# Kernel tuning notes

Hardware: AMD Instinct MI355X
Metric: run time of the kernel (lower is better)

The kernel has to match this reference:

```python
import jax, jax.numpy as jnp
import numpy as np

B, N_CGS, N_ATOMS, KNN, K, DEPTH = 16, 256, 1024, 32, 128, 3
CUTOFF = 10.0


def _init_params(key):
    ks = jax.random.split(key, 12)
    s = 1.0 / np.sqrt(K)
    p = {}
    # stacked per-depth settransform weights: Linear stored as [in, out] (y = x @ W + b)
    p['mlp_W1'] = jax.random.normal(ks[0], (DEPTH, K, K), jnp.float32) * s
    p['mlp_b1'] = jnp.zeros((DEPTH, K), jnp.float32)
    p['mlp_W2'] = jax.random.normal(ks[1], (DEPTH, K, K), jnp.float32) * s
    p['mlp_b2'] = jnp.zeros((DEPTH, K), jnp.float32)
    p['upd_W1'] = jax.random.normal(ks[2], (DEPTH, K, K), jnp.float32) * s
    p['upd_b1'] = jnp.zeros((DEPTH, K), jnp.float32)
    p['upd_W2'] = jax.random.normal(ks[3], (DEPTH, K, K), jnp.float32) * s
    p['upd_b2'] = jnp.zeros((DEPTH, K), jnp.float32)
    p['dec_W1'] = jax.random.normal(ks[4], (K, K), jnp.float32) * s
    p['dec_b1'] = jnp.zeros((K,), jnp.float32)
    p['dec_W2'] = jax.random.normal(ks[5], (K, N_ATOMS), jnp.float32) * s
    p['dec_b2'] = jnp.zeros((N_ATOMS,), jnp.float32)
    return p


def setup_inputs() -> dict:
    key = jax.random.key(0)
    ks = jax.random.split(key, 6)
    inp = {
        'soft_assign': jax.random.uniform(ks[0], (B, N_ATOMS, N_CGS), jnp.float32),
        'xyz': jax.random.normal(ks[1], (B, N_ATOMS, 3), jnp.float32),
        'cg_xyz': jax.random.normal(ks[2], (B, N_CGS, 3), jnp.float32),
        'assign_norm': jax.random.uniform(ks[3], (B, N_ATOMS, N_CGS), jnp.float32),
        'assign_idx': jax.random.randint(ks[4], (N_ATOMS,), 0, N_CGS, jnp.int32),
    }
    inp.update(_init_params(ks[5]))
    return inp


def _forward(cg_xyz, assign_norm, assign_idx,
             mlp_W1, mlp_b1, mlp_W2, mlp_b2,
             upd_W1, upd_b1, upd_W2, upd_b2,
             dec_W1, dec_b1, dec_W2, dec_b2):
    act = jax.nn.relu
    # Pairwise CG distance + ascending sort (as in source). The source then
    # zeroes sorted values beyond rank knn and uses value.nonzero()[:, 1:] as
    # neighbor pairs, i.e. it indexes by SORT RANK (ranks 1..knn), not by the
    # sorted index tensor knbrs. For generic (distinct) coordinates this is
    # exactly: neighbor j in {1..knn} for every center i. We replicate that.
    dist_vec = cg_xyz[:, None, 1:KNN + 1, :] - cg_xyz[:, :, None, :]  # [B, n_cgs, knn, 3]
    dist_vec = dist_vec.reshape(B, N_CGS * KNN, 3)
    dist = jnp.sqrt(jnp.sum(dist_vec ** 2, axis=-1)).reshape(B, N_CGS, KNN, 1)

    # GaussianSmearing(0, cutoff, feature_dim)
    offset = jnp.linspace(0.0, CUTOFF, K)  # [K]
    coeff = -0.5 / (offset[1] - offset[0]) ** 2
    out = jnp.exp(coeff * (dist - offset) ** 2)  # [B, n_cgs, knn, K]

    # settransform layers (loop over small fixed depth)
    for d in range(DEPTH):
        upd = act(out @ mlp_W1[d] + mlp_b1[d]) @ mlp_W2[d] + mlp_b2[d]
        cg_contract = jnp.mean(upd, axis=-2, keepdims=True)  # mean over knn axis
        h = upd + cg_contract
        out = act(h @ upd_W1[d] + upd_b1[d]) @ upd_W2[d] + upd_b2[d]

    # decode K -> n_atoms
    coeffs = (act(out @ dec_W1 + dec_b1) @ dec_W2 + dec_b2)
    coeffs = coeffs.reshape(B, N_CGS * KNN, N_ATOMS)

    dx_recon = jnp.einsum('bio,bin->bon', coeffs, dist_vec)      # [B, n_atoms, 3]
    cg_offset = jnp.einsum('bin,bij->bjn', dx_recon, assign_norm)  # [B, n_cgs, 3]
    cg_offset_lift = cg_offset[:, assign_idx, :]                  # [B, n_atoms, 3]
    xyz_recon = cg_xyz[:, assign_idx, :] - cg_offset_lift + dx_recon
    return xyz_recon


def reference(soft_assign, xyz, cg_xyz, assign_norm, assign_idx,
              mlp_W1, mlp_b1, mlp_W2, mlp_b2,
              upd_W1, upd_b1, upd_W2, upd_b2,
              dec_W1, dec_b1, dec_W2, dec_b2):
    xyz_recon = _forward(cg_xyz, assign_norm, assign_idx,
                         mlp_W1, mlp_b1, mlp_W2, mlp_b2,
                         upd_W1, upd_b1, upd_W2, upd_b2,
                         dec_W1, dec_b1, dec_W2, dec_b2)
    return (soft_assign, xyz, xyz_recon)
```

## Files before the change

kernel.cpp:

```cpp
#include <hip/hip_runtime.h>

#define BATCH   16
#define NCGS    256
#define NATOMS  1024
#define KNN     32
#define KF      128
#define NSLICE  8

typedef __attribute__((ext_vector_type(8))) short bf16x8;
typedef __attribute__((ext_vector_type(4))) float f32x4;

#define NFRAG (13*8*4)

union U16B { bf16x8 v; uint u[4]; };

__global__ __launch_bounds__(256)
void prep_kernel(const float* __restrict__ mlp_W1, const float* __restrict__ mlp_W2,
                 const float* __restrict__ upd_W1, const float* __restrict__ upd_W2,
                 const float* __restrict__ dec_W1, uint* __restrict__ Wswz)
{
    int t = blockIdx.x * 256 + threadIdx.x;
    if (t >= 13*8*4*64) return;
    int lane = t & 63;
    int kc   = (t >> 6) & 3;
    int ft   = (t >> 8) & 7;
    int s    = t >> 11;

    const float* W;
    if (s < 12) {
        int d = s >> 2, ph = s & 3;
        if      (ph == 0) W = mlp_W1 + d*KF*KF;
        else if (ph == 1) W = mlp_W2 + d*KF*KF;
        else if (ph == 2) W = upd_W1 + d*KF*KF;
        else              W = upd_W2 + d*KF*KF;
    } else W = dec_W1;

    int f = ft*16 + (lane & 15);
    int g = lane >> 4;

    uint hi[4], lo[4];
    #pragma unroll
    for (int w = 0; w < 4; ++w) {
        int k0;
        if (s == 0) k0 = kc*32 + g*8 + 2*w;
        else        k0 = kc*16 + (w>>1)*64 + g*4 + 2*(w&1);
        float v0 = W[(size_t)k0*KF + f];
        float v1 = W[(size_t)(k0+1)*KF + f];
        uint b0 = __float_as_uint(v0), b1 = __float_as_uint(v1);
        hi[w] = (b0 >> 16) | (b1 & 0xffff0000u);
        float l0 = v0 - __uint_as_float(b0 & 0xffff0000u);
        float l1 = v1 - __uint_as_float(b1 & 0xffff0000u);
        lo[w] = (__float_as_uint(l0) >> 16) | (__float_as_uint(l1) & 0xffff0000u);
    }
    int fi = (s*8 + ft)*4 + kc;
    uint* ph_ = Wswz + (size_t)((fi*2 + 0)*64 + lane)*4;
    uint* pl_ = Wswz + (size_t)((fi*2 + 1)*64 + lane)*4;
    #pragma unroll
    for (int w = 0; w < 4; ++w) { ph_[w] = hi[w]; pl_[w] = lo[w]; }
}

template<int KC, int FH>
__device__ __forceinline__ void loadw(bf16x8 (&wb)[8], const bf16x8* __restrict__ Ws, int l)
{
    #pragma unroll
    for (int i = 0; i < 4; ++i) {
        const int idx = ((FH*4 + i)*4 + KC)*2;
        wb[i*2+0] = Ws[(idx+0)*64 + l];
        wb[i*2+1] = Ws[(idx+1)*64 + l];
    }
}

template<int KC, int FH>
__device__ __forceinline__ void compw(const bf16x8 (&wb)[8],
        const bf16x8 (&bh)[2][4], const bf16x8 (&bl)[2][4], f32x4 (&acc)[8][2])
{
    #pragma unroll
    for (int i = 0; i < 4; ++i) {
        const int ft = FH*4 + i;
        bf16x8 whi = wb[i*2+0], wlo = wb[i*2+1];
        #pragma unroll
        for (int rt = 0; rt < 2; ++rt) {
            acc[ft][rt] = __builtin_amdgcn_mfma_f32_16x16x32_bf16(whi, bh[rt][KC], acc[ft][rt], 0, 0, 0);
            acc[ft][rt] = __builtin_amdgcn_mfma_f32_16x16x32_bf16(whi, bl[rt][KC], acc[ft][rt], 0, 0, 0);
            acc[ft][rt] = __builtin_amdgcn_mfma_f32_16x16x32_bf16(wlo, bh[rt][KC], acc[ft][rt], 0, 0, 0);
        }
    }
}

__global__ __launch_bounds__(256, 2)
void mlp_kernel(const float* __restrict__ cg_xyz, const bf16x8* __restrict__ Wf,
                const float* __restrict__ mlp_b1, const float* __restrict__ mlp_b2,
                const float* __restrict__ upd_b1, const float* __restrict__ upd_b2,
                const float* __restrict__ dec_b1, float* __restrict__ Gp)
{
    const int tid = threadIdx.x;
    const int wv  = tid >> 6;
    const int l   = tid & 63;
    const int g   = l >> 4;
    const int e0  = l & 15;
    const int b   = blockIdx.x >> 6;
    const int cg  = (blockIdx.x & 63) * 4 + wv;

    const float* cgb = cg_xyz + (size_t)b * NCGS * 3;
    const float cx = cgb[cg*3+0], cy = cgb[cg*3+1], cz = cgb[cg*3+2];
    const float d0x = cgb[(1+e0)*3+0]-cx,  d0y = cgb[(1+e0)*3+1]-cy,  d0z = cgb[(1+e0)*3+2]-cz;
    const float d1x = cgb[(17+e0)*3+0]-cx, d1y = cgb[(17+e0)*3+1]-cy, d1z = cgb[(17+e0)*3+2]-cz;
    const float dist0 = sqrtf(d0x*d0x + d0y*d0y + d0z*d0z);
    const float dist1 = sqrtf(d1x*d1x + d1y*d1y + d1z*d1z);

    const float STEP  = 10.0f / 127.0f;
    const float COEFF = -0.5f / (STEP * STEP);
    bf16x8 bh[2][4], bl[2][4];
    #pragma unroll
    for (int rt = 0; rt < 2; ++rt) {
        float dd = rt ? dist1 : dist0;
        #pragma unroll
        for (int kc = 0; kc < 4; ++kc) {
            U16B H, L;
            #pragma unroll
            for (int w = 0; w < 4; ++w) {
                int k0 = kc*32 + g*8 + 2*w;
                float t0 = dd - (float)k0 * STEP;
                float t1 = dd - (float)(k0+1) * STEP;
                float e0f = __expf(COEFF * t0 * t0);
                float e1f = __expf(COEFF * t1 * t1);
                uint b0 = __float_as_uint(e0f), b1 = __float_as_uint(e1f);
                H.u[w] = (b0 >> 16) | (b1 & 0xffff0000u);
                float l0 = e0f - __uint_as_float(b0 & 0xffff0000u);
                float l1 = e1f - __uint_as_float(b1 & 0xffff0000u);
                L.u[w] = (__float_as_uint(l0) >> 16) | (__float_as_uint(l1) & 0xffff0000u);
            }
            bh[rt][kc] = H.v; bl[rt][kc] = L.v;
        }
    }

    f32x4 acc[8][2];
    bf16x8 wb0[8], wb1[8];
    for (int s = 0; s < 13; ++s) {
        const float* bias; int md;
        if (s < 12) {
            int d = s >> 2, ph = s & 3;
            if      (ph == 0) { bias = mlp_b1 + d*KF; md = 0; }
            else if (ph == 1) { bias = mlp_b2 + d*KF; md = 1; }
            else if (ph == 2) { bias = upd_b1 + d*KF; md = 0; }
            else              { bias = upd_b2 + d*KF; md = 2; }
        } else { bias = dec_b1; md = 0; }

        const bf16x8* Ws = Wf + (size_t)(s*8)*4*2*64;

        loadw<0,0>(wb0, Ws, l);

        #pragma unroll
        for (int ft = 0; ft < 8; ++ft) {
            float4 bv = *(const float4*)(bias + ft*16 + g*4);
            acc[ft][0] = (f32x4){bv.x, bv.y, bv.z, bv.w};
            acc[ft][1] = acc[ft][0];
        }

        loadw<0,1>(wb1, Ws, l);  compw<0,0>(wb0, bh, bl, acc);
        loadw<1,0>(wb0, Ws, l);  compw<0,1>(wb1, bh, bl, acc);
        loadw<1,1>(wb1, Ws, l);  compw<1,0>(wb0, bh, bl, acc);
        loadw<2,0>(wb0, Ws, l);  compw<1,1>(wb1, bh, bl, acc);
        loadw<2,1>(wb1, Ws, l);  compw<2,0>(wb0, bh, bl, acc);
        loadw<3,0>(wb0, Ws, l);  compw<2,1>(wb1, bh, bl, acc);
        loadw<3,1>(wb1, Ws, l);  compw<3,0>(wb0, bh, bl, acc);
                                 compw<3,1>(wb1, bh, bl, acc);

        if (md == 0) {
            #pragma unroll
            for (int ft = 0; ft < 8; ++ft)
                #pragma unroll
                for (int rt = 0; rt < 2; ++rt)
                    #pragma unroll
                    for (int q = 0; q < 4; ++q)
                        acc[ft][rt][q] = fmaxf(acc[ft][rt][q], 0.f);
        } else if (md == 1) {
            #pragma unroll
            for (int ft = 0; ft < 8; ++ft)
                #pragma unroll
                for (int q = 0; q < 4; ++q) {
                    float sm = acc[ft][0][q] + acc[ft][1][q];
                    sm += __shfl_xor(sm, 1);
                    sm += __shfl_xor(sm, 2);
                    sm += __shfl_xor(sm, 4);
                    sm += __shfl_xor(sm, 8);
                    float mn = sm * (1.0f / 32.0f);
                    acc[ft][0][q] += mn;
                    acc[ft][1][q] += mn;
                }
        }

        if (s < 12) {
            #pragma unroll
            for (int rt = 0; rt < 2; ++rt)
                #pragma unroll
                for (int kc = 0; kc < 4; ++kc) {
                    float v0 = acc[kc  ][rt][0], v1 = acc[kc  ][rt][1];
                    float v2 = acc[kc  ][rt][2], v3 = acc[kc  ][rt][3];
                    float v4 = acc[kc+4][rt][0], v5 = acc[kc+4][rt][1];
                    float v6 = acc[kc+4][rt][2], v7 = acc[kc+4][rt][3];
                    uint u0=__float_as_uint(v0), u1=__float_as_uint(v1);
                    uint u2=__float_as_uint(v2), u3=__float_as_uint(v3);
                    uint u4=__float_as_uint(v4), u5=__float_as_uint(v5);
                    uint u6=__float_as_uint(v6), u7=__float_as_uint(v7);
                    U16B H, L;
                    H.u[0] = (u0>>16)|(u1&0xffff0000u);
                    H.u[1] = (u2>>16)|(u3&0xffff0000u);
                    H.u[2] = (u4>>16)|(u5&0xffff0000u);
                    H.u[3] = (u6>>16)|(u7&0xffff0000u);
                    float l0=v0-__uint_as_float(u0&0xffff0000u), l1=v1-__uint_as_float(u1&0xffff0000u);
                    float l2=v2-__uint_as_float(u2&0xffff0000u), l3=v3-__uint_as_float(u3&0xffff0000u);
                    float l4=v4-__uint_as_float(u4&0xffff0000u), l5=v5-__uint_as_float(u5&0xffff0000u);
                    float l6=v6-__uint_as_float(u6&0xffff0000u), l7=v7-__uint_as_float(u7&0xffff0000u);
                    L.u[0] = (__float_as_uint(l0)>>16)|(__float_as_uint(l1)&0xffff0000u);
                    L.u[1] = (__float_as_uint(l2)>>16)|(__float_as_uint(l3)&0xffff0000u);
                    L.u[2] = (__float_as_uint(l4)>>16)|(__float_as_uint(l5)&0xffff0000u);
                    L.u[3] = (__float_as_uint(l6)>>16)|(__float_as_uint(l7)&0xffff0000u);
                    bh[rt][kc] = H.v; bl[rt][kc] = L.v;
                }
        }
    }

    const int slice = blockIdx.x & (NSLICE-1);
    float* Gb = Gp + ((size_t)slice*BATCH + b) * KF * 3;
    #pragma unroll
    for (int ft = 0; ft < 8; ++ft) {
        #pragma unroll
        for (int q = 0; q < 4; ++q) {
            float r0 = acc[ft][0][q], r1 = acc[ft][1][q];
            float px = r0*d0x + r1*d1x;
            float py = r0*d0y + r1*d1y;
            float pz = r0*d0z + r1*d1z;
            px += __shfl_xor(px, 1); py += __shfl_xor(py, 1); pz += __shfl_xor(pz, 1);
            px += __shfl_xor(px, 2); py += __shfl_xor(py, 2); pz += __shfl_xor(pz, 2);
            px += __shfl_xor(px, 4); py += __shfl_xor(py, 4); pz += __shfl_xor(pz, 4);
            px += __shfl_xor(px, 8); py += __shfl_xor(py, 8); pz += __shfl_xor(pz, 8);
            if (e0 < 3) {
                float pv = (e0 == 0) ? px : ((e0 == 1) ? py : pz);
                atomicAdd(Gb + (16*ft + 4*g + q)*3 + e0, pv);
            }
        }
    }
}

__global__ __launch_bounds__(256)
void dx_kernel(const float* __restrict__ cg_xyz, const float* __restrict__ dec_W2,
               const float* __restrict__ dec_b2, const float* __restrict__ Gp,
               float* __restrict__ dxr)
{
    __shared__ float Gl[KF * 3];
    __shared__ float red[256 * 3];
    const int tid = threadIdx.x;
    const int b   = blockIdx.x >> 2;
    const int og  = blockIdx.x & 3;

    if (tid < 192) {
        float s0 = 0.f, s1 = 0.f;
        #pragma unroll
        for (int sl = 0; sl < NSLICE; ++sl) {
            const float* gp = Gp + ((size_t)sl*BATCH + b) * KF * 3;
            s0 += gp[tid]; s1 += gp[tid + 192];
        }
        Gl[tid] = s0; Gl[tid + 192] = s1;
    }
    const float* cgb = cg_xyz + (size_t)b * NCGS * 3;
    float w = ((tid >= 1 && tid <= 32) ? 256.f : 0.f) - 32.f;
    red[tid]       = w * cgb[tid*3+0];
    red[256 + tid] = w * cgb[tid*3+1];
    red[512 + tid] = w * cgb[tid*3+2];
    __syncthreads();
    for (int s2 = 128; s2 > 0; s2 >>= 1) {
        if (tid < s2) {
            red[tid]       += red[tid + s2];
            red[256 + tid] += red[256 + tid + s2];
            red[512 + tid] += red[512 + tid + s2];
        }
        __syncthreads();
    }
    const float S0 = red[0], S1 = red[256], S2 = red[512];

    const int o = og * 256 + tid;
    const float bq = dec_b2[o];
    float a0 = bq * S0, a1 = bq * S1, a2 = bq * S2;
    #pragma unroll 4
    for (int k = 0; k < KF; ++k) {
        float wvv = dec_W2[k * NATOMS + o];
        a0 = fmaf(wvv, Gl[k*3+0], a0);
        a1 = fmaf(wvv, Gl[k*3+1], a1);
        a2 = fmaf(wvv, Gl[k*3+2], a2);
    }
    float* dp = dxr + ((size_t)b * NATOMS + o) * 3;
    dp[0] = a0; dp[1] = a1; dp[2] = a2;
}

__global__ __launch_bounds__(256)
void cgo_kernel(const float* __restrict__ assign_norm, const float* __restrict__ dxr,
                float* __restrict__ cgo)
{
    __shared__ float dxl[64 * 3];
    const int tid = threadIdx.x;
    const int b   = blockIdx.x >> 4;
    const int a0  = (blockIdx.x & 15) * 64;
    if (tid < 192) dxl[tid] = dxr[((size_t)b * NATOMS + a0) * 3 + tid];
    __syncthreads();
    float c0 = 0.f, c1 = 0.f, c2 = 0.f;
    const float* an = assign_norm + ((size_t)b * NATOMS + a0) * NCGS + tid;
    #pragma unroll 4
    for (int a = 0; a < 64; ++a) {
        float v = an[(size_t)a * NCGS];
        c0 = fmaf(v, dxl[a*3+0], c0);
        c1 = fmaf(v, dxl[a*3+1], c1);
        c2 = fmaf(v, dxl[a*3+2], c2);
    }
    float* cp = cgo + ((size_t)b * NCGS + tid) * 3;
    atomicAdd(cp+0, c0); atomicAdd(cp+1, c1); atomicAdd(cp+2, c2);
}

__global__ __launch_bounds__(256)
void recon_kernel(const float* __restrict__ cg_xyz, const float* __restrict__ cgo,
                  const float* __restrict__ dxr, const int* __restrict__ assign_idx,
                  float* __restrict__ out)
{
    int i = blockIdx.x * 256 + threadIdx.x;
    int b   = i / (NATOMS * 3);
    int rem = i - b * (NATOMS * 3);
    int a   = rem / 3;
    int n   = rem - a * 3;
    int ia  = assign_idx[a];
    float v = cg_xyz[((size_t)b*NCGS + ia)*3 + n]
            - cgo[((size_t)b*NCGS + ia)*3 + n]
            + dxr[((size_t)b*NATOMS + a)*3 + n];
    out[i] = v;
}

extern "C" void kernel_launch(void* const* d_in, const int* in_sizes, int n_in,
                              void* d_out, int out_size, void* d_ws, size_t ws_size,
                              hipStream_t stream)
{
    const float* soft_assign = (const float*)d_in[0];
    const float* xyz         = (const float*)d_in[1];
    const float* cg_xyz      = (const float*)d_in[2];
    const float* assign_norm = (const float*)d_in[3];
    const int*   assign_idx  = (const int*)  d_in[4];
    const float* mlp_W1 = (const float*)d_in[5];
    const float* mlp_b1 = (const float*)d_in[6];
    const float* mlp_W2 = (const float*)d_in[7];
    const float* mlp_b2 = (const float*)d_in[8];
    const float* upd_W1 = (const float*)d_in[9];
    const float* upd_b1 = (const float*)d_in[10];
    const float* upd_W2 = (const float*)d_in[11];
    const float* upd_b2 = (const float*)d_in[12];
    const float* dec_W1 = (const float*)d_in[13];
    const float* dec_b1 = (const float*)d_in[14];
    const float* dec_W2 = (const float*)d_in[15];
    const float* dec_b2 = (const float*)d_in[16];

    float* out = (float*)d_out;

    uint*  Wswz = (uint*)d_ws;
    float* Gp   = (float*)d_ws + NFRAG*2*64*4;
    float* cgo  = Gp + NSLICE * BATCH * KF * 3;
    float* dxr  = cgo + BATCH * NCGS * 3;

    hipMemcpyAsync(out, soft_assign, (size_t)BATCH*NATOMS*NCGS*sizeof(float),
                   hipMemcpyDeviceToDevice, stream);
    hipMemcpyAsync(out + (size_t)BATCH*NATOMS*NCGS, xyz,
                   (size_t)BATCH*NATOMS*3*sizeof(float),
                   hipMemcpyDeviceToDevice, stream);
    hipMemsetAsync(Gp, 0,
        (size_t)(NSLICE*BATCH*KF*3 + BATCH*NCGS*3)*sizeof(float), stream);

    prep_kernel<<<104, 256, 0, stream>>>(mlp_W1, mlp_W2, upd_W1, upd_W2, dec_W1, Wswz);
    mlp_kernel<<<BATCH*64, 256, 0, stream>>>(cg_xyz, (const bf16x8*)Wswz,
        mlp_b1, mlp_b2, upd_b1, upd_b2, dec_b1, Gp);
    dx_kernel<<<BATCH*4, 256, 0, stream>>>(cg_xyz, dec_W2, dec_b2, Gp, dxr);
    cgo_kernel<<<BATCH*16, 256, 0, stream>>>(assign_norm, dxr, cgo);
    recon_kernel<<<(BATCH*NATOMS*3)/256, 256, 0, stream>>>(
        cg_xyz, cgo, dxr, assign_idx,
        out + (size_t)BATCH*NATOMS*NCGS + (size_t)BATCH*NATOMS*3);
}
```

Before: 357.6 us.

## Stage MLP weights into double-buffered LDS via async global-to-LDS loads

```diff
diff --git a/kernel.cpp b/kernel.cpp
--- a/kernel.cpp
+++ b/kernel.cpp
@@ -59,25 +59,36 @@
     for (int w = 0; w < 4; ++w) { ph_[w] = hi[w]; pl_[w] = lo[w]; }
 }
 
+__device__ __forceinline__ void gload_lds16(const void* g, void* l)
+{
+    __builtin_amdgcn_global_load_lds(
+        (const __attribute__((address_space(1))) void*)g,
+        (__attribute__((address_space(3))) void*)l, 16, 0, 0);
+}
+
+__device__ __forceinline__ void stage_half(const char* __restrict__ Wbase,
+                                           int s, int hf, char* buf, int wv, int l)
+{
+    #pragma unroll
+    for (int q = 0; q < 8; ++q) {
+        int j   = wv*8 + q;
+        int kc2 = j >> 4, ft = (j >> 1) & 7, p = j & 1;
+        int fi  = (s*8 + ft)*4 + (2*hf + kc2);
+        const char* g = Wbase + ((size_t)(fi*2 + p))*1024 + (size_t)l*16;
+        gload_lds16(g, buf + (size_t)j*1024);
+    }
+}
+
 template<int KC, int FH>
-__device__ __forceinline__ void loadw(bf16x8 (&wb)[8], const bf16x8* __restrict__ Ws, int l)
-{
-    #pragma unroll
-    for (int i = 0; i < 4; ++i) {
-        const int idx = ((FH*4 + i)*4 + KC)*2;
-        wb[i*2+0] = Ws[(idx+0)*64 + l];
-        wb[i*2+1] = Ws[(idx+1)*64 + l];
-    }
-}
-
-template<int KC, int FH>
-__device__ __forceinline__ void compw(const bf16x8 (&wb)[8],
+__device__ __forceinline__ void comp_grp(const char* buf, int l,
         const bf16x8 (&bh)[2][4], const bf16x8 (&bl)[2][4], f32x4 (&acc)[8][2])
 {
+    constexpr int KC2 = KC & 1;
     #pragma unroll
     for (int i = 0; i < 4; ++i) {
         const int ft = FH*4 + i;
-        bf16x8 whi = wb[i*2+0], wlo = wb[i*2+1];
+        bf16x8 whi = *(const bf16x8*)(buf + (size_t)(((KC2*8 + ft)*2 + 0)*1024) + (size_t)l*16);
+        bf16x8 wlo = *(const bf16x8*)(buf + (size_t)(((KC2*8 + ft)*2 + 1)*1024) + (size_t)l*16);
         #pragma unroll
         for (int rt = 0; rt < 2; ++rt) {
             acc[ft][rt] = __builtin_amdgcn_mfma_f32_16x16x32_bf16(whi, bh[rt][KC], acc[ft][rt], 0, 0, 0);
@@ -88,11 +99,13 @@
 }
 
 __global__ __launch_bounds__(256, 2)
-void mlp_kernel(const float* __restrict__ cg_xyz, const bf16x8* __restrict__ Wf,
+void mlp_kernel(const float* __restrict__ cg_xyz, const char* __restrict__ Wf,
                 const float* __restrict__ mlp_b1, const float* __restrict__ mlp_b2,
                 const float* __restrict__ upd_b1, const float* __restrict__ upd_b2,
                 const float* __restrict__ dec_b1, float* __restrict__ Gp)
 {
+    __shared__ __align__(16) char Wlds[2][32*1024];
+
     const int tid = threadIdx.x;
     const int wv  = tid >> 6;
     const int l   = tid & 63;
@@ -100,6 +113,8 @@
     const int e0  = l & 15;
     const int b   = blockIdx.x >> 6;
     const int cg  = (blockIdx.x & 63) * 4 + wv;
+
+    stage_half(Wf, 0, 0, Wlds[0], wv, l);
 
     const float* cgb = cg_xyz + (size_t)b * NCGS * 3;
     const float cx = cgb[cg*3+0], cy = cgb[cg*3+1], cz = cgb[cg*3+2];
@@ -134,21 +149,22 @@
         }
     }
 
+    asm volatile("s_waitcnt vmcnt(0)" ::: "memory");
+    __syncthreads();
+
     f32x4 acc[8][2];
-    bf16x8 wb0[8], wb1[8];
     for (int s = 0; s < 13; ++s) {
         const float* bias; int md;
-        if (s < 12) {
+        {
             int d = s >> 2, ph = s & 3;
-            if      (ph == 0) { bias = mlp_b1 + d*KF; md = 0; }
-            else if (ph == 1) { bias = mlp_b2 + d*KF; md = 1; }
-            else if (ph == 2) { bias = upd_b1 + d*KF; md = 0; }
-            else              { bias = upd_b2 + d*KF; md = 2; }
-        } else { bias = dec_b1; md = 0; }
-
-        const bf16x8* Ws = Wf + (size_t)(s*8)*4*2*64;
-
-        loadw<0,0>(wb0, Ws, l);
+            if      (s == 12)  { bias = dec_b1;        md = 0; }
+            else if (ph == 0)  { bias = mlp_b1 + d*KF; md = 0; }
+            else if (ph == 1)  { bias = mlp_b2 + d*KF; md = 1; }
+            else if (ph == 2)  { bias = upd_b1 + d*KF; md = 0; }
+            else               { bias = upd_b2 + d*KF; md = 2; }
+        }
+
+        stage_half(Wf, s, 1, Wlds[1], wv, l);
 
         #pragma unroll
         for (int ft = 0; ft < 8; ++ft) {
@@ -157,14 +173,20 @@
             acc[ft][1] = acc[ft][0];
         }
 
-        loadw<0,1>(wb1, Ws, l);  compw<0,0>(wb0, bh, bl, acc);
-        loadw<1,0>(wb0, Ws, l);  compw<0,1>(wb1, bh, bl, acc);
-        loadw<1,1>(wb1, Ws, l);  compw<1,0>(wb0, bh, bl, acc);
-        loadw<2,0>(wb0, Ws, l);  compw<1,1>(wb1, bh, bl, acc);
-        loadw<2,1>(wb1, Ws, l);  compw<2,0>(wb0, bh, bl, acc);
-        loadw<3,0>(wb0, Ws, l);  compw<2,1>(wb1, bh, bl, acc);
-        loadw<3,1>(wb1, Ws, l);  compw<3,0>(wb0, bh, bl, acc);
-                                 compw<3,1>(wb1, bh, bl, acc);
+        comp_grp<0,0>(Wlds[0], l, bh, bl, acc);
+        comp_grp<0,1>(Wlds[0], l, bh, bl, acc);
+        comp_grp<1,0>(Wlds[0], l, bh, bl, acc);
+        comp_grp<1,1>(Wlds[0], l, bh, bl, acc);
+
+        asm volatile("s_waitcnt vmcnt(0)" ::: "memory");
+        __syncthreads();
+
+        if (s < 12) stage_half(Wf, s+1, 0, Wlds[0], wv, l);
+
+        comp_grp<2,0>(Wlds[1], l, bh, bl, acc);
+        comp_grp<2,1>(Wlds[1], l, bh, bl, acc);
+        comp_grp<3,0>(Wlds[1], l, bh, bl, acc);
+        comp_grp<3,1>(Wlds[1], l, bh, bl, acc);
 
         if (md == 0) {
             #pragma unroll
@@ -219,6 +241,9 @@
                     bh[rt][kc] = H.v; bl[rt][kc] = L.v;
                 }
         }
+
+        asm volatile("s_waitcnt vmcnt(0)" ::: "memory");
+        __syncthreads();
     }
 
     const int slice = blockIdx.x & (NSLICE-1);
@@ -371,7 +396,7 @@
         (size_t)(NSLICE*BATCH*KF*3 + BATCH*NCGS*3)*sizeof(float), stream);
 
     prep_kernel<<<104, 256, 0, stream>>>(mlp_W1, mlp_W2, upd_W1, upd_W2, dec_W1, Wswz);
-    mlp_kernel<<<BATCH*64, 256, 0, stream>>>(cg_xyz, (const bf16x8*)Wswz,
+    mlp_kernel<<<BATCH*64, 256, 0, stream>>>(cg_xyz, (const char*)Wswz,
         mlp_b1, mlp_b2, upd_b1, upd_b2, dec_b1, Gp);
     dx_kernel<<<BATCH*4, 256, 0, stream>>>(cg_xyz, dec_W2, dec_b2, Gp, dxr);
     cgo_kernel<<<BATCH*16, 256, 0, stream>>>(assign_norm, dxr, cgo);
```

New measurement: 301.2 us. -15.8%, faster.
